# Kernel tuning notes

Measured on AMD Instinct MI355X. Metric: run time of the kernel, lower is better.

## Reference

```python
import jax, jax.numpy as jnp
import numpy as np

B, T, D = 4, 4096, 1024
HD = 64              # head_dim
H = D // HD          # n_heads = 16
C = 64               # chunk_size (T % C == 0)


def setup_inputs() -> dict:
    key = jax.random.key(0)
    k1, k2, k3 = jax.random.split(key, 3)
    out = jax.random.normal(k1, (B, T, D), jnp.float32)
    # Linear(d_model, d_model, bias=False) weights, ~1/sqrt(D) scale
    W_write = jax.random.normal(k2, (D, D), jnp.float32) * 0.03
    W_read = jax.random.normal(k3, (D, D), jnp.float32) * 0.03
    decay = jnp.full((H,), 4.6, jnp.float32)                 # torch init value
    log_alpha = jnp.log(jnp.full((H,), 0.03, jnp.float32))   # memory_alpha=0.03
    return {"out": out, "W_write": W_write, "W_read": W_read,
            "decay": decay, "log_alpha": log_alpha}


def reference(out, W_write, W_read, decay, log_alpha):
    Bb, Tt, Dd = out.shape
    d, Hh, Cc = HD, D // HD, C
    out32 = out.astype(jnp.float32)
    gamma = jax.nn.sigmoid(decay)          # (H,)
    log_gamma = jnp.log(gamma)

    # projections and head split: (B, H, T, d)
    v = (out32 @ W_write.T).reshape(Bb, Tt, Hh, d).transpose(0, 2, 1, 3)
    rk = out32.reshape(Bb, Tt, Hh, d).transpose(0, 2, 1, 3)
    wk = jnp.pad(rk[:, :, :-1], ((0, 0), (0, 0), (1, 0), (0, 0)))  # shift right by 1

    BH = Bb * Hh
    gamma_bh = jnp.tile(gamma, Bb)          # (BH,) index b*H+h -> gamma[h]
    log_gamma_bh = jnp.tile(log_gamma, Bb)
    nC = Tt // Cc
    # (nC, BH, C, d) so lax.scan runs over chunks
    v_ch = v.reshape(BH, nC, Cc, d).transpose(1, 0, 2, 3)
    rk_ch = rk.reshape(BH, nC, Cc, d).transpose(1, 0, 2, 3)
    wk_ch = wk.reshape(BH, nC, Cc, d).transpose(1, 0, 2, 3)

    p = jnp.arange(Cc)
    diffs = jnp.clip(p[:, None] - 1 - p[None, :], 0)          # (C, C)
    causal = p[:, None] > p[None, :]
    # per-(b,h) intra-chunk decay mask (BH, C, C)
    M = jnp.exp(diffs[None].astype(jnp.float32) * log_gamma_bh[:, None, None]) * causal[None]
    g_p = gamma_bh[:, None] ** p[None, :].astype(jnp.float32)            # (BH, C)
    g_w = gamma_bh[:, None] ** (Cc - 1 - p)[None, :].astype(jnp.float32)  # (BH, C)
    g_C = gamma_bh ** Cc                                                  # (BH,)

    def scan_fn(W, chunk):
        rk_c, wk_c, v_c = chunk                                   # each (BH, C, d)
        inter = jnp.einsum('bij,bcj->bci', W, rk_c) * g_p[:, :, None]
        S = jnp.einsum('bcd,bkd->bck', rk_c, wk_c)                # (BH, C, C)
        intra = jnp.einsum('bck,bkd->bcd', S * M, v_c)
        W_new = g_C[:, None, None] * W + jnp.einsum('bci,bcj->bij', v_c * g_w[:, :, None], wk_c)
        return W_new, inter + intra

    W0 = jnp.zeros((BH, d, d), jnp.float32)
    _, reads = jax.lax.scan(scan_fn, W0, (rk_ch, wk_ch, v_ch))   # (nC, BH, C, d)
    reads = reads.transpose(1, 0, 2, 3).reshape(Bb, Hh, Tt, d)
    alpha = jnp.exp(log_alpha)[None, :, None, None]
    reads = (alpha * reads).transpose(0, 2, 1, 3).reshape(Bb, Tt, Dd)
    return out + (reads @ W_read.T).astype(out.dtype)
```

## Files before the change

kernel.cpp:

```cpp
#include <hip/hip_runtime.h>
#include <hip/hip_bf16.h>
#include <stdint.h>


typedef __bf16 bf16x8 __attribute__((ext_vector_type(8)));
typedef float f32x4 __attribute__((ext_vector_type(4)));

#define GAS __attribute__((address_space(1)))
#define LAS __attribute__((address_space(3)))

__device__ __forceinline__ unsigned short f2bf(float f) {
  unsigned u = __float_as_uint(f);
  u = (u + 0x7fffu + ((u >> 16) & 1u)) >> 16;
  return (unsigned short)u;
}
__device__ __forceinline__ float bf2f(unsigned short h) {
  return __uint_as_float(((unsigned)h) << 16);
}

__global__ __launch_bounds__(256) void cast_f32_to_bf16(
    const float* __restrict__ src, unsigned short* __restrict__ dst, int n8) {
  int i = blockIdx.x * 256 + threadIdx.x;
  if (i >= n8) return;
  const float4* s = (const float4*)src + (size_t)i * 2;
  float4 f0 = s[0], f1 = s[1];
  union { uint4 u4; unsigned short us[8]; } o;
  o.us[0] = f2bf(f0.x); o.us[1] = f2bf(f0.y); o.us[2] = f2bf(f0.z); o.us[3] = f2bf(f0.w);
  o.us[4] = f2bf(f1.x); o.us[5] = f2bf(f1.y); o.us[6] = f2bf(f1.z); o.us[7] = f2bf(f1.w);
  ((uint4*)dst)[i] = o.u4;
}

__global__ __launch_bounds__(256) void gemm_bt_bf16out(
    const unsigned short* __restrict__ A, const unsigned short* __restrict__ B,
    unsigned short* __restrict__ C, int M, int N, int K) {
  __shared__ unsigned short As[128 * 32];
  __shared__ unsigned short Bs[128 * 32];
  int tid = threadIdx.x;
  int l = tid & 63, w = tid >> 6;
  int bm = blockIdx.y, bn = blockIdx.x;
  int wm = (w >> 1) * 64, wn = (w & 1) * 64;
  f32x4 acc[4][4];
#pragma unroll
  for (int mi = 0; mi < 4; mi++)
#pragma unroll
    for (int ni = 0; ni < 4; ni++) acc[mi][ni] = (f32x4){0.f, 0.f, 0.f, 0.f};
  const unsigned short* Ab = A + (size_t)bm * 128 * K;
  const unsigned short* Bb = B + (size_t)bn * 128 * K;
  int lr = l >> 2, lc = (l & 3) * 8;
  int lm = l & 15, q4 = l >> 4;
  for (int k0 = 0; k0 < K; k0 += 32) {
#pragma unroll
    for (int q = 0; q < 2; q++) {
      int g = (w * 2 + q) * 16 + lr;
      __builtin_amdgcn_global_load_lds((GAS void*)(void*)(Ab + (size_t)g * K + k0 + lc),
                                       (LAS void*)(&As[(w * 2 + q) * 512]), 16, 0, 0);
      __builtin_amdgcn_global_load_lds((GAS void*)(void*)(Bb + (size_t)g * K + k0 + lc),
                                       (LAS void*)(&Bs[(w * 2 + q) * 512]), 16, 0, 0);
    }
    __syncthreads();
    bf16x8 a[4], b[4];
#pragma unroll
    for (int mi = 0; mi < 4; mi++) a[mi] = *(const bf16x8*)&As[(wm + mi * 16 + lm) * 32 + q4 * 8];
#pragma unroll
    for (int ni = 0; ni < 4; ni++) b[ni] = *(const bf16x8*)&Bs[(wn + ni * 16 + lm) * 32 + q4 * 8];
#pragma unroll
    for (int mi = 0; mi < 4; mi++)
#pragma unroll
      for (int ni = 0; ni < 4; ni++)
        acc[mi][ni] = __builtin_amdgcn_mfma_f32_16x16x32_bf16(a[mi], b[ni], acc[mi][ni], 0, 0, 0);
    __syncthreads();
  }
#pragma unroll
  for (int mi = 0; mi < 4; mi++)
#pragma unroll
    for (int ni = 0; ni < 4; ni++) {
      int r0 = bm * 128 + wm + mi * 16 + q4 * 4;
      int col = bn * 128 + wn + ni * 16 + lm;
#pragma unroll
      for (int j = 0; j < 4; j++)
        C[(size_t)(r0 + j) * N + col] = f2bf(acc[mi][ni][j]);
    }
}

__global__ __launch_bounds__(256) void gemm_bt_addout(
    const unsigned short* __restrict__ A, const unsigned short* __restrict__ B,
    const float* __restrict__ base, float* __restrict__ C, int M, int N, int K) {
  __shared__ unsigned short As[128 * 32];
  __shared__ unsigned short Bs[128 * 32];
  int tid = threadIdx.x;
  int l = tid & 63, w = tid >> 6;
  int bm = blockIdx.y, bn = blockIdx.x;
  int wm = (w >> 1) * 64, wn = (w & 1) * 64;
  f32x4 acc[4][4];
#pragma unroll
  for (int mi = 0; mi < 4; mi++)
#pragma unroll
    for (int ni = 0; ni < 4; ni++) acc[mi][ni] = (f32x4){0.f, 0.f, 0.f, 0.f};
  const unsigned short* Ab = A + (size_t)bm * 128 * K;
  const unsigned short* Bb = B + (size_t)bn * 128 * K;
  int lr = l >> 2, lc = (l & 3) * 8;
  int lm = l & 15, q4 = l >> 4;
  for (int k0 = 0; k0 < K; k0 += 32) {
#pragma unroll
    for (int q = 0; q < 2; q++) {
      int g = (w * 2 + q) * 16 + lr;
      __builtin_amdgcn_global_load_lds((GAS void*)(void*)(Ab + (size_t)g * K + k0 + lc),
                                       (LAS void*)(&As[(w * 2 + q) * 512]), 16, 0, 0);
      __builtin_amdgcn_global_load_lds((GAS void*)(void*)(Bb + (size_t)g * K + k0 + lc),
                                       (LAS void*)(&Bs[(w * 2 + q) * 512]), 16, 0, 0);
    }
    __syncthreads();
    bf16x8 a[4], b[4];
#pragma unroll
    for (int mi = 0; mi < 4; mi++) a[mi] = *(const bf16x8*)&As[(wm + mi * 16 + lm) * 32 + q4 * 8];
#pragma unroll
    for (int ni = 0; ni < 4; ni++) b[ni] = *(const bf16x8*)&Bs[(wn + ni * 16 + lm) * 32 + q4 * 8];
#pragma unroll
    for (int mi = 0; mi < 4; mi++)
#pragma unroll
      for (int ni = 0; ni < 4; ni++)
        acc[mi][ni] = __builtin_amdgcn_mfma_f32_16x16x32_bf16(a[mi], b[ni], acc[mi][ni], 0, 0, 0);
    __syncthreads();
  }
#pragma unroll
  for (int mi = 0; mi < 4; mi++)
#pragma unroll
    for (int ni = 0; ni < 4; ni++) {
      int r0 = bm * 128 + wm + mi * 16 + q4 * 4;
      int col = bn * 128 + wn + ni * 16 + lm;
#pragma unroll
      for (int j = 0; j < 4; j++) {
        size_t ad = (size_t)(r0 + j) * N + col;
        C[ad] = base[ad] + acc[mi][ni][j];
      }
    }
}

__global__ __launch_bounds__(256) void chunk_local(
    const unsigned short* __restrict__ rkg,
    const unsigned short* __restrict__ vg,
    const float* __restrict__ decay,
    unsigned short* __restrict__ intra_bf,
    unsigned short* __restrict__ U_bf) {
  int c = blockIdx.x, bh = blockIdx.y;
  int b = bh >> 4, h = bh & 15;
  int tid = threadIdx.x, l = tid & 63, w = tid >> 6;
  float gamma = 1.0f / (1.0f + __expf(-decay[h]));
  float lg = __logf(gamma);

  __shared__ unsigned short rk_s[64 * 72];
  __shared__ unsigned short wk_s[64 * 72];
  __shared__ unsigned short wkT_s[64 * 72];
  __shared__ unsigned short vT_s[64 * 72];
  __shared__ unsigned short S_s[64 * 72];

  const size_t rowbase = (((size_t)b * 4096 + (size_t)c * 64) * 1024) + h * 64;

#pragma unroll
  for (int r = 0; r < 2; r++) {
    int e = r * 256 + tid;
    int p = e >> 3, seg = e & 7;
    uint4 dr = *(const uint4*)(rkg + rowbase + (size_t)p * 1024 + seg * 8);
    *(uint4*)&rk_s[p * 72 + seg * 8] = dr;
    uint4 dv = *(const uint4*)(vg + rowbase + (size_t)p * 1024 + seg * 8);
    {
      unsigned uu[4] = {dv.x, dv.y, dv.z, dv.w};
#pragma unroll
      for (int qq = 0; qq < 4; qq++) {
        vT_s[(seg * 8 + qq * 2) * 72 + p] = (unsigned short)(uu[qq] & 0xffffu);
        vT_s[(seg * 8 + qq * 2 + 1) * 72 + p] = (unsigned short)(uu[qq] >> 16);
      }
    }
    int tg = c * 64 + p - 1;
    uint4 dw = make_uint4(0u, 0u, 0u, 0u);
    if (tg >= 0) dw = *(const uint4*)(rkg + ((size_t)b * 4096 + tg) * 1024 + h * 64 + seg * 8);
    *(uint4*)&wk_s[p * 72 + seg * 8] = dw;
    {
      unsigned uu[4] = {dw.x, dw.y, dw.z, dw.w};
#pragma unroll
      for (int qq = 0; qq < 4; qq++) {
        wkT_s[(seg * 8 + qq * 2) * 72 + p] = (unsigned short)(uu[qq] & 0xffffu);
        wkT_s[(seg * 8 + qq * 2 + 1) * 72 + p] = (unsigned short)(uu[qq] >> 16);
      }
    }
  }
  __syncthreads();

  int lm = l & 15, q4 = l >> 4;

  {
    bf16x8 a0 = *(const bf16x8*)&rk_s[(w * 16 + lm) * 72 + q4 * 8];
    bf16x8 a1 = *(const bf16x8*)&rk_s[(w * 16 + lm) * 72 + 32 + q4 * 8];
#pragma unroll
    for (int ni = 0; ni < 4; ni++) {
      bf16x8 b0 = *(const bf16x8*)&wk_s[(ni * 16 + lm) * 72 + q4 * 8];
      bf16x8 b1 = *(const bf16x8*)&wk_s[(ni * 16 + lm) * 72 + 32 + q4 * 8];
      f32x4 acc = {0.f, 0.f, 0.f, 0.f};
      acc = __builtin_amdgcn_mfma_f32_16x16x32_bf16(a0, b0, acc, 0, 0, 0);
      acc = __builtin_amdgcn_mfma_f32_16x16x32_bf16(a1, b1, acc, 0, 0, 0);
#pragma unroll
      for (int j = 0; j < 4; j++) {
        int p = w * 16 + q4 * 4 + j;
        int q = ni * 16 + lm;
        float m = (p > q) ? __expf(lg * (float)(p - 1 - q)) : 0.0f;
        S_s[p * 72 + q] = f2bf(acc[j] * m);
      }
    }
  }
  __syncthreads();

  {
    bf16x8 a0 = *(const bf16x8*)&S_s[(w * 16 + lm) * 72 + q4 * 8];
    bf16x8 a1 = *(const bf16x8*)&S_s[(w * 16 + lm) * 72 + 32 + q4 * 8];
#pragma unroll
    for (int ni = 0; ni < 4; ni++) {
      bf16x8 b0 = *(const bf16x8*)&vT_s[(ni * 16 + lm) * 72 + q4 * 8];
      bf16x8 b1 = *(const bf16x8*)&vT_s[(ni * 16 + lm) * 72 + 32 + q4 * 8];
      f32x4 acc = {0.f, 0.f, 0.f, 0.f};
      acc = __builtin_amdgcn_mfma_f32_16x16x32_bf16(a0, b0, acc, 0, 0, 0);
      acc = __builtin_amdgcn_mfma_f32_16x16x32_bf16(a1, b1, acc, 0, 0, 0);
#pragma unroll
      for (int j = 0; j < 4; j++) {
        int p = w * 16 + q4 * 4 + j;
        int i = ni * 16 + lm;
        intra_bf[rowbase + (size_t)p * 1024 + i] = f2bf(acc[j]);
      }
    }
  }

  {
    bf16x8 a0 = *(const bf16x8*)&vT_s[(w * 16 + lm) * 72 + q4 * 8];
    bf16x8 a1 = *(const bf16x8*)&vT_s[(w * 16 + lm) * 72 + 32 + q4 * 8];
#pragma unroll
    for (int jj = 0; jj < 8; jj++) {
      int p0 = q4 * 8 + jj;
      a0[jj] = (__bf16)((float)a0[jj] * __expf(lg * (float)(63 - p0)));
      a1[jj] = (__bf16)((float)a1[jj] * __expf(lg * (float)(63 - (p0 + 32))));
    }
    size_t ub = ((size_t)bh * 64 + c) * 4096;
#pragma unroll
    for (int nj = 0; nj < 4; nj++) {
      bf16x8 b0 = *(const bf16x8*)&wkT_s[(nj * 16 + lm) * 72 + q4 * 8];
      bf16x8 b1 = *(const bf16x8*)&wkT_s[(nj * 16 + lm) * 72 + 32 + q4 * 8];
      f32x4 acc = {0.f, 0.f, 0.f, 0.f};
      acc = __builtin_amdgcn_mfma_f32_16x16x32_bf16(a0, b0, acc, 0, 0, 0);
      acc = __builtin_amdgcn_mfma_f32_16x16x32_bf16(a1, b1, acc, 0, 0, 0);
#pragma unroll
      for (int j = 0; j < 4; j++) {
        int i = w * 16 + q4 * 4 + j;
        int col = nj * 16 + lm;
        U_bf[ub + i * 64 + col] = f2bf(acc[j]);
      }
    }
  }
}

__global__ __launch_bounds__(256) void scan_states(
    const unsigned short* __restrict__ U_bf, unsigned short* __restrict__ Wst,
    const float* __restrict__ decay) {
  int bh = blockIdx.x, h = bh & 15, tid = threadIdx.x;
  float gamma = 1.0f / (1.0f + __expf(-decay[h]));
  float gC = __expf(64.0f * __logf(gamma));
  float Wr[16];
#pragma unroll
  for (int r = 0; r < 16; r++) Wr[r] = 0.f;
  size_t base = (size_t)bh * 64 * 4096;
  for (int c = 0; c < 64; c++) {
    size_t o = base + (size_t)c * 4096;
#pragma unroll
    for (int r = 0; r < 16; r++) {
      Wst[o + r * 256 + tid] = f2bf(Wr[r]);
      Wr[r] = gC * Wr[r] + bf2f(U_bf[o + r * 256 + tid]);
    }
  }
}

__global__ __launch_bounds__(256) void inter_combine(
    const unsigned short* __restrict__ rkg, const unsigned short* __restrict__ Wst,
    const unsigned short* __restrict__ intra_bf,
    const float* __restrict__ decay, const float* __restrict__ log_alpha,
    unsigned short* __restrict__ reads_bf) {
  int c = blockIdx.x, bh = blockIdx.y;
  int b = bh >> 4, h = bh & 15;
  int tid = threadIdx.x, l = tid & 63, w = tid >> 6;
  float gamma = 1.0f / (1.0f + __expf(-decay[h]));
  float lg = __logf(gamma);
  float alpha = __expf(log_alpha[h]);
  __shared__ unsigned short rk_s[64 * 72];
  __shared__ unsigned short W_s[64 * 72];
  const size_t rowbase = (((size_t)b * 4096 + (size_t)c * 64) * 1024) + h * 64;
  size_t wbase = ((size_t)bh * 64 + c) * 4096;
#pragma unroll
  for (int r = 0; r < 2; r++) {
    int e = r * 256 + tid;
    int p = e >> 3, seg = e & 7;
    *(uint4*)&rk_s[p * 72 + seg * 8] = *(const uint4*)(rkg + rowbase + (size_t)p * 1024 + seg * 8);
    *(uint4*)&W_s[p * 72 + seg * 8] = *(const uint4*)(Wst + wbase + (size_t)e * 8);
  }
  __syncthreads();
  int lm = l & 15, q4 = l >> 4;
  bf16x8 a0 = *(const bf16x8*)&rk_s[(w * 16 + lm) * 72 + q4 * 8];
  bf16x8 a1 = *(const bf16x8*)&rk_s[(w * 16 + lm) * 72 + 32 + q4 * 8];
#pragma unroll
  for (int ni = 0; ni < 4; ni++) {
    bf16x8 b0 = *(const bf16x8*)&W_s[(ni * 16 + lm) * 72 + q4 * 8];
    bf16x8 b1 = *(const bf16x8*)&W_s[(ni * 16 + lm) * 72 + 32 + q4 * 8];
    f32x4 acc = {0.f, 0.f, 0.f, 0.f};
    acc = __builtin_amdgcn_mfma_f32_16x16x32_bf16(a0, b0, acc, 0, 0, 0);
    acc = __builtin_amdgcn_mfma_f32_16x16x32_bf16(a1, b1, acc, 0, 0, 0);
#pragma unroll
    for (int j = 0; j < 4; j++) {
      int p = w * 16 + q4 * 4 + j;
      int i = ni * 16 + lm;
      float gp = __expf(lg * (float)p);
      size_t ad = rowbase + (size_t)p * 1024 + i;
      reads_bf[ad] = f2bf(alpha * (acc[j] * gp + bf2f(intra_bf[ad])));
    }
  }
}

extern "C" void kernel_launch(void* const* d_in, const int* in_sizes, int n_in,
                              void* d_out, int out_size, void* d_ws, size_t ws_size,
                              hipStream_t stream) {
  const float* out_f = (const float*)d_in[0];
  const float* Ww = (const float*)d_in[1];
  const float* Wr = (const float*)d_in[2];
  const float* decay = (const float*)d_in[3];
  const float* lalpha = (const float*)d_in[4];

  char* ws = (char*)d_ws;
  unsigned short* outbf = (unsigned short*)(ws + 0);
  unsigned short* vbf   = (unsigned short*)(ws + 33554432);
  unsigned short* wwbf  = (unsigned short*)(ws + 67108864);
  unsigned short* wrbf  = (unsigned short*)(ws + 69206016);
  unsigned short* intra = (unsigned short*)(ws + 71303168);
  unsigned short* U     = (unsigned short*)(ws + 104857600);
  unsigned short* Wst   = (unsigned short*)(ws + 138412032);
  unsigned short* reads = (unsigned short*)(ws + 171966464);

  cast_f32_to_bf16<<<dim3(8192), 256, 0, stream>>>(out_f, outbf, 16777216 / 8);
  cast_f32_to_bf16<<<dim3(512), 256, 0, stream>>>(Ww, wwbf, 1048576 / 8);
  cast_f32_to_bf16<<<dim3(512), 256, 0, stream>>>(Wr, wrbf, 1048576 / 8);

  gemm_bt_bf16out<<<dim3(8, 128), 256, 0, stream>>>(outbf, wwbf, vbf, 16384, 1024, 1024);

  chunk_local<<<dim3(64, 64), 256, 0, stream>>>(outbf, vbf, decay, intra, U);
  scan_states<<<dim3(64), 256, 0, stream>>>(U, Wst, decay);
  inter_combine<<<dim3(64, 64), 256, 0, stream>>>(outbf, Wst, intra, decay, lalpha, reads);

  gemm_bt_addout<<<dim3(8, 128), 256, 0, stream>>>(reads, wrbf, out_f, (float*)d_out,
                                                   16384, 1024, 1024);
}
```

Baseline: 339.8 us.

## Replace sequential state scan with decay-matrix MFMA matmul and swizzle GEMM tiles

The per-head serial scan over 64 chunks, launched as only 64 blocks, is replaced by a lower-triangular decay matrix L[c,k]=gC^(c-1-k) multiplied against the chunk updates U with MFMA. This spreads the state computation across 2048 blocks instead of a serial loop. Both projection GEMMs now use a 1D grid with an 8x8 block swizzle to improve L2 reuse of A and B tiles. The matmul form rounds the decay weights to bf16 and accumulates in a different order, so numerics shift slightly.

```diff
diff --git a/kernel.cpp b/kernel.cpp
--- a/kernel.cpp
+++ b/kernel.cpp
@@ -30,6 +30,13 @@
   ((uint4*)dst)[i] = o.u4;
 }
 
+__device__ __forceinline__ void swizzle_bm_bn(int id, int& bm, int& bn) {
+  int x = id & 7;
+  int s = id >> 3;
+  bn = s & 7;
+  bm = ((s >> 3) << 3) | x;
+}
+
 __global__ __launch_bounds__(256) void gemm_bt_bf16out(
     const unsigned short* __restrict__ A, const unsigned short* __restrict__ B,
     unsigned short* __restrict__ C, int M, int N, int K) {
@@ -37,7 +44,8 @@
   __shared__ unsigned short Bs[128 * 32];
   int tid = threadIdx.x;
   int l = tid & 63, w = tid >> 6;
-  int bm = blockIdx.y, bn = blockIdx.x;
+  int bm, bn;
+  swizzle_bm_bn(blockIdx.x, bm, bn);
   int wm = (w >> 1) * 64, wn = (w & 1) * 64;
   f32x4 acc[4][4];
 #pragma unroll
@@ -89,7 +97,8 @@
   __shared__ unsigned short Bs[128 * 32];
   int tid = threadIdx.x;
   int l = tid & 63, w = tid >> 6;
-  int bm = blockIdx.y, bn = blockIdx.x;
+  int bm, bn;
+  swizzle_bm_bn(blockIdx.x, bm, bn);
   int wm = (w >> 1) * 64, wn = (w & 1) * 64;
   f32x4 acc[4][4];
 #pragma unroll
@@ -255,24 +264,73 @@
   }
 }
 
-__global__ __launch_bounds__(256) void scan_states(
+__global__ __launch_bounds__(256) void scan_matmul(
     const unsigned short* __restrict__ U_bf, unsigned short* __restrict__ Wst,
     const float* __restrict__ decay) {
-  int bh = blockIdx.x, h = bh & 15, tid = threadIdx.x;
+  int col0 = blockIdx.x * 128, bh = blockIdx.y, h = bh & 15;
+  int tid = threadIdx.x, l = tid & 63, w = tid >> 6;
   float gamma = 1.0f / (1.0f + __expf(-decay[h]));
-  float gC = __expf(64.0f * __logf(gamma));
-  float Wr[16];
-#pragma unroll
-  for (int r = 0; r < 16; r++) Wr[r] = 0.f;
-  size_t base = (size_t)bh * 64 * 4096;
-  for (int c = 0; c < 64; c++) {
-    size_t o = base + (size_t)c * 4096;
-#pragma unroll
-    for (int r = 0; r < 16; r++) {
-      Wst[o + r * 256 + tid] = f2bf(Wr[r]);
-      Wr[r] = gC * Wr[r] + bf2f(U_bf[o + r * 256 + tid]);
-    }
-  }
+  float lgC = 64.0f * __logf(gamma);
+
+  __shared__ unsigned short L_s[64 * 72];
+  __shared__ unsigned short B_s[128 * 72];
+
+  {
+    int m = tid >> 2, kk0 = (tid & 3) * 16;
+#pragma unroll
+    for (int e = 0; e < 16; e++) {
+      int k = kk0 + e;
+      float v = (k < m) ? __expf(lgC * (float)(m - 1 - k)) : 0.0f;
+      L_s[m * 72 + k] = f2bf(v);
+    }
+  }
+  size_t ub = (size_t)bh * 64 * 4096 + col0;
+#pragma unroll
+  for (int it = 0; it < 4; it++) {
+    int e = it * 256 + tid;
+    int k = e >> 4, seg = e & 15;
+    uint4 d = *(const uint4*)(U_bf + ub + (size_t)k * 4096 + seg * 8);
+    unsigned uu[4] = {d.x, d.y, d.z, d.w};
+#pragma unroll
+    for (int qq = 0; qq < 4; qq++) {
+      B_s[(seg * 8 + qq * 2) * 72 + k] = (unsigned short)(uu[qq] & 0xffffu);
+      B_s[(seg * 8 + qq * 2 + 1) * 72 + k] = (unsigned short)(uu[qq] >> 16);
+    }
+  }
+  __syncthreads();
+
+  int lm = l & 15, q4 = l >> 4;
+  f32x4 acc[4][2];
+#pragma unroll
+  for (int mi = 0; mi < 4; mi++)
+#pragma unroll
+    for (int ni = 0; ni < 2; ni++) acc[mi][ni] = (f32x4){0.f, 0.f, 0.f, 0.f};
+#pragma unroll
+  for (int kk = 0; kk < 2; kk++) {
+    bf16x8 a[4], b[2];
+#pragma unroll
+    for (int mi = 0; mi < 4; mi++)
+      a[mi] = *(const bf16x8*)&L_s[(mi * 16 + lm) * 72 + kk * 32 + q4 * 8];
+#pragma unroll
+    for (int ni = 0; ni < 2; ni++)
+      b[ni] = *(const bf16x8*)&B_s[(w * 32 + ni * 16 + lm) * 72 + kk * 32 + q4 * 8];
+#pragma unroll
+    for (int mi = 0; mi < 4; mi++)
+#pragma unroll
+      for (int ni = 0; ni < 2; ni++)
+        acc[mi][ni] = __builtin_amdgcn_mfma_f32_16x16x32_bf16(a[mi], b[ni], acc[mi][ni], 0, 0, 0);
+  }
+  size_t wb = (size_t)bh * 64 * 4096 + col0;
+#pragma unroll
+  for (int mi = 0; mi < 4; mi++)
+#pragma unroll
+    for (int ni = 0; ni < 2; ni++)
+#pragma unroll
+      for (int j = 0; j < 4; j++) {
+        int c = mi * 16 + q4 * 4 + j;
+        int n = w * 32 + ni * 16 + lm;
+        Wst[wb + (size_t)c * 4096 + n] = f2bf(acc[mi][ni][j]);
+      }
 }
 
 __global__ __launch_bounds__(256) void inter_combine(
@@ -342,12 +400,12 @@
   cast_f32_to_bf16<<<dim3(512), 256, 0, stream>>>(Ww, wwbf, 1048576 / 8);
   cast_f32_to_bf16<<<dim3(512), 256, 0, stream>>>(Wr, wrbf, 1048576 / 8);
 
-  gemm_bt_bf16out<<<dim3(8, 128), 256, 0, stream>>>(outbf, wwbf, vbf, 16384, 1024, 1024);
+  gemm_bt_bf16out<<<dim3(1024), 256, 0, stream>>>(outbf, wwbf, vbf, 16384, 1024, 1024);
 
   chunk_local<<<dim3(64, 64), 256, 0, stream>>>(outbf, vbf, decay, intra, U);
-  scan_states<<<dim3(64), 256, 0, stream>>>(U, Wst, decay);
+  scan_matmul<<<dim3(32, 64), 256, 0, stream>>>(U, Wst, decay);
   inter_combine<<<dim3(64, 64), 256, 0, stream>>>(outbf, Wst, intra, decay, lalpha, reads);
 
-  gemm_bt_addout<<<dim3(8, 128), 256, 0, stream>>>(reads, wrbf, out_f, (float*)d_out,
-                                                   16384, 1024, 1024);
-}
+  gemm_bt_addout<<<dim3(1024), 256, 0, stream>>>(reads, wrbf, out_f, (float*)d_out,
+                                                 16384, 1024, 1024);
+}
```

Result: faster. 321.3 us (-5.4%).
